# Optimization experiments

Measured on AMD Instinct MI355X. Metric: run time of the kernel, lower is better.

The kernel has to match this reference:

```python
import jax, jax.numpy as jnp
import numpy as np

B, C_IN, C_OUT = 2, 32, 32
N_IN = 128 * 128            # input grid points
N_OUT = 128 * 128           # output grid points
KERNEL_SIZE = 9             # (3-1)*4 + 1 for kernel_shape=[3,4], piecewise_linear basis
NNZ = 1_500_000             # sparse entries in psi (kernel_size, n_out, n_in)


def setup_inputs() -> dict:
    key = jax.random.key(0)
    ks = jax.random.split(key, 8)
    scale = (1.0 / C_IN) ** 0.5  # sqrt(1/groupsize), groups=1
    return {
        "x": jax.random.normal(ks[0], (B, C_IN, N_IN), jnp.float32),
        "quadrature_weights": jax.random.uniform(ks[1], (N_IN,), jnp.float32, 0.5, 1.5) / N_IN,
        "psi_vals": jax.random.uniform(ks[2], (NNZ,), jnp.float32),
        "weight": scale * jax.random.normal(ks[3], (C_OUT, C_IN, KERNEL_SIZE), jnp.float32),
        "bias": jnp.zeros((C_OUT,), jnp.float32),
        "psi_idx_k": jax.random.randint(ks[4], (NNZ,), 0, KERNEL_SIZE, dtype=jnp.int32),
        "psi_idx_out": jax.random.randint(ks[5], (NNZ,), 0, N_OUT, dtype=jnp.int32),
        "psi_idx_in": jax.random.randint(ks[6], (NNZ,), 0, N_IN, dtype=jnp.int32),
        "n_out": N_OUT,
    }


def reference(x, quadrature_weights, psi_vals, weight, bias,
              psi_idx_k, psi_idx_out, psi_idx_in, n_out):
    # x: (B, C, n_in); weight: (O, C, K); psi is sparse (K, n_out, n_in)
    Bb, C, n_in = x.shape
    K = weight.shape[2]
    # pre-multiply by quadrature weights, layout (n_in, B, C) for gather
    xq = (x * quadrature_weights[None, None, :]).transpose(2, 0, 1)
    # gather-weight: contribution of each sparse entry  -> (nnz, B, C)
    contrib = xq[psi_idx_in] * psi_vals[:, None, None]
    # scatter-add into (kernel, out) bins == sparse psi @ xq
    seg = psi_idx_k * n_out + psi_idx_out
    xk = jax.ops.segment_sum(contrib, seg, num_segments=K * n_out)
    xk = xk.reshape(K, n_out, Bb, C)  # (K, n_out, B, C)
    # channel/kernel mixing with learned weight (groups=1)
    out = jnp.einsum("knbc,ock->bon", xk, weight) + bias[None, :, None]
    return out  # (B, out_channels, n_out)
```

## Files before the change

kernel.cpp:

```cpp
#include <hip/hip_runtime.h>

#define N_IN   16384
#define N_OUT  16384
#define KSZ    9
#define CIN    32
#define COUT   32
#define BC     64
#define NBUCK  1024
#define TNB    16
#define CHUNK  4096
#define ROWS   (KSZ * TNB)
#define XSTR   64
#define ECAP   2048

__global__ void k_xq(const float* __restrict__ x, const float* __restrict__ qw,
                     float* __restrict__ xq) {
    __shared__ float tile[64 * 65];
    const int in0 = blockIdx.x * 64;
    const int tid = threadIdx.x;
#pragma unroll
    for (int i = 0; i < 16; ++i) {
        int idx = tid + i * 256;
        int bcl = idx >> 6, inl = idx & 63;
        tile[bcl * 65 + inl] = x[bcl * N_IN + in0 + inl];
    }
    __syncthreads();
#pragma unroll
    for (int i = 0; i < 16; ++i) {
        int idx = tid + i * 256;
        int inl = idx >> 6, bcl = idx & 63;
        xq[(size_t)(in0 + inl) * BC + bcl] = tile[bcl * 65 + inl] * qw[in0 + inl];
    }
}

__global__ void k_wt(const float* __restrict__ w, float* __restrict__ wT) {
    int i = blockIdx.x * 256 + threadIdx.x;
    if (i < COUT * CIN * KSZ) {
        int o = i / (CIN * KSZ);
        int r = i - o * (CIN * KSZ);
        int c = r / KSZ;
        int k = r - c * KSZ;
        wT[((k * 8 + (o >> 2)) * 32 + c) * 4 + (o & 3)] = w[i];
    }
}

__global__ __launch_bounds__(512) void k_bin(const float* __restrict__ vals,
        const int* __restrict__ ik, const int* __restrict__ io, const int* __restrict__ ii,
        int* __restrict__ gcnt, float2* __restrict__ siv, int nnz) {
    __shared__ int cnt[NBUCK];
    __shared__ int cur[NBUCK];
    __shared__ int lim[NBUCK];
    const int t = threadIdx.x, c = blockIdx.x;
    cnt[t] = 0; cnt[t + 512] = 0;
    __syncthreads();
    const int base = c * CHUNK;
    int iov[8];
#pragma unroll
    for (int j = 0; j < 8; ++j) {
        int e = base + j * 512 + t;
        iov[j] = (e < nnz) ? io[e] : -1;
        if (iov[j] >= 0) atomicAdd(&cnt[iov[j] >> 4], 1);
    }
    __syncthreads();
#pragma unroll
    for (int s = 0; s < NBUCK; s += 512) {
        int b = t + s;
        int cb = cnt[b];
        int rs = cb ? atomicAdd(&gcnt[b], cb) : 0;
        int avail = min(cb, max(0, ECAP - rs));
        cur[b] = b * ECAP + rs;
        lim[b] = b * ECAP + rs + avail;
    }
    __syncthreads();
#pragma unroll
    for (int j = 0; j < 8; ++j) {
        int e = base + j * 512 + t;
        if (iov[j] >= 0) {
            int o = iov[j], b = o >> 4;
            int packed = (ii[e] << 8) | (ik[e] * TNB + (o & (TNB - 1)));
            int pos = atomicAdd(&cur[b], 1);
            if (pos < lim[b]) siv[pos] = make_float2(vals[e], __int_as_float(packed));
        }
    }
}

__global__ __launch_bounds__(512) void k_fused3(const float* __restrict__ xq,
        const float2* __restrict__ siv, const int* __restrict__ gcnt,
        const float* __restrict__ wT, const float* __restrict__ bias,
        float* __restrict__ out) {
    __shared__ float  sxk[ROWS * XSTR];
    __shared__ float2 slist[ECAP];
    __shared__ int    rowStart[ROWS + 1];
    __shared__ int    cursor[ROWS];
    const int tid  = threadIdx.x;
    const int lane = tid & 63;
    const int wv   = __builtin_amdgcn_readfirstlane(tid >> 6);
    const int bkt  = blockIdx.x;

    for (int i = tid; i < ROWS * XSTR; i += 512) sxk[i] = 0.f;
    if (tid < ROWS) rowStart[tid] = 0;
    __syncthreads();

    const int m = min(gcnt[bkt], ECAP);
    const float2* src = siv + (size_t)bkt * ECAP;
    float2 ent[4]; bool have[4];
#pragma unroll
    for (int j = 0; j < 4; ++j) {
        int i = tid + j * 512;
        have[j] = (i < m);
        if (have[j]) {
            ent[j] = src[i];
            atomicAdd(&rowStart[__float_as_int(ent[j].y) & 0xFF], 1);
        }
    }
    __syncthreads();
    if (wv == 0) {
        int carry = 0;
#pragma unroll
        for (int i0 = 0; i0 < 192; i0 += 64) {
            int idx = i0 + lane;
            int v = (idx < ROWS) ? rowStart[idx] : 0;
            int orig = v;
#pragma unroll
            for (int off = 1; off < 64; off <<= 1) {
                int u = __shfl_up(v, off);
                if (lane >= off) v += u;
            }
            if (idx < ROWS) {
                int excl = carry + v - orig;
                rowStart[idx] = excl;
                cursor[idx]   = excl;
            }
            carry += __shfl(v, 63);
        }
        if (lane == 0) rowStart[ROWS] = m;
    }
    __syncthreads();
#pragma unroll
    for (int j = 0; j < 4; ++j) {
        if (have[j]) {
            int pos = atomicAdd(&cursor[__float_as_int(ent[j].y) & 0xFF], 1);
            slist[pos] = ent[j];
        }
    }
    __syncthreads();
    const char* xqb   = (const char*)xq;
    const int   lane4 = lane * 4;
    for (int r = wv; r < ROWS; r += 8) {
        const int a = rowStart[r], b = rowStart[r + 1];
        if (a == b) continue;
        float acc0 = 0.f, acc1 = 0.f, acc2 = 0.f, acc3 = 0.f;
        int i = a;
        for (; i + 3 < b; i += 4) {
            float2 v0 = slist[i], v1 = slist[i + 1], v2 = slist[i + 2], v3 = slist[i + 3];
            int o0 = (__float_as_int(v0.y) & 0x3FFF00) + lane4;
            int o1 = (__float_as_int(v1.y) & 0x3FFF00) + lane4;
            int o2 = (__float_as_int(v2.y) & 0x3FFF00) + lane4;
            int o3 = (__float_as_int(v3.y) & 0x3FFF00) + lane4;
            acc0 += *(const float*)(xqb + o0) * v0.x;
            acc1 += *(const float*)(xqb + o1) * v1.x;
            acc2 += *(const float*)(xqb + o2) * v2.x;
            acc3 += *(const float*)(xqb + o3) * v3.x;
        }
        for (; i < b; ++i) {
            float2 v = slist[i];
            int o = (__float_as_int(v.y) & 0x3FFF00) + lane4;
            acc0 += *(const float*)(xqb + o) * v.x;
        }
        sxk[r * XSTR + lane] = (acc0 + acc1) + (acc2 + acc3);
    }
    __syncthreads();

    if (lane < 32) {
        const int h  = lane >> 4;
        const int nl = lane & 15;
        const int n0 = bkt * TNB;
        float acc[4] = {0.f, 0.f, 0.f, 0.f};
        for (int k = 0; k < KSZ; ++k) {
            const float* xr = &sxk[(k * TNB + nl) * XSTR + h * 32];
            const float* wp = &wT[(k * 8 + wv) * 128];
#pragma unroll
            for (int c4 = 0; c4 < 8; ++c4) {
                float4 xv = *(const float4*)&xr[c4 * 4];
#pragma unroll
                for (int cc = 0; cc < 4; ++cc) {
                    float xval = (&xv.x)[cc];
#pragma unroll
                    for (int j = 0; j < 4; ++j)
                        acc[j] += xval * wp[(c4 * 4 + cc) * 4 + j];
                }
            }
        }
#pragma unroll
        for (int j = 0; j < 4; ++j) {
            int o = wv * 4 + j;
            out[((size_t)h * COUT + o) * N_OUT + n0 + nl] = acc[j] + bias[o];
        }
    }
}

extern "C" void kernel_launch(void* const* d_in, const int* in_sizes, int n_in,
                              void* d_out, int out_size, void* d_ws, size_t ws_size,
                              hipStream_t stream) {
    const float* x    = (const float*)d_in[0];
    const float* qw   = (const float*)d_in[1];
    const float* vals = (const float*)d_in[2];
    const float* w    = (const float*)d_in[3];
    const float* bias = (const float*)d_in[4];
    const int*   ik   = (const int*)d_in[5];
    const int*   io   = (const int*)d_in[6];
    const int*   ii   = (const int*)d_in[7];
    const int    nnz  = in_sizes[2];
    const int    nch  = (nnz + CHUNK - 1) / CHUNK;

    char* ws = (char*)d_ws;
    float*  xq   = (float*)ws;  ws += (size_t)N_IN * BC * 4;
    float2* siv  = (float2*)ws; ws += (size_t)NBUCK * ECAP * 8;
    int*    gcnt = (int*)ws;    ws += (size_t)NBUCK * 4;
    float*  wT   = (float*)ws;  ws += (size_t)COUT * CIN * KSZ * 4;

    hipMemsetAsync(gcnt, 0, (size_t)NBUCK * 4, stream);
    k_xq <<<N_IN / 64, 256, 0, stream>>>(x, qw, xq);
    k_wt <<<(COUT * CIN * KSZ + 255) / 256, 256, 0, stream>>>(w, wT);
    k_bin<<<nch, 512, 0, stream>>>(vals, ik, io, ii, gcnt, siv, nnz);
    k_fused3<<<NBUCK, 512, 0, stream>>>(xq, siv, gcnt, wT, bias, (float*)d_out);
}
```

Before: 184.2 us.

## Merge prep kernels, stage bucketed entries in LDS, vectorize binning loads

```diff
diff --git a/kernel.cpp b/kernel.cpp
--- a/kernel.cpp
+++ b/kernel.cpp
@@ -10,14 +10,26 @@
 #define TNB    16
 #define CHUNK  4096
 #define ROWS   (KSZ * TNB)
-#define XSTR   64
+#define XSTR   68
 #define ECAP   2048
 
 __global__ void k_xq(const float* __restrict__ x, const float* __restrict__ qw,
-                     float* __restrict__ xq) {
+                     float* __restrict__ xq, const float* __restrict__ w,
+                     float* __restrict__ wT, int* __restrict__ gcnt) {
+    const int tid = threadIdx.x;
+    if (blockIdx.x == 256) {
+        for (int i = tid; i < COUT * CIN * KSZ; i += 256) {
+            int o = i / (CIN * KSZ);
+            int r = i - o * (CIN * KSZ);
+            int c = r / KSZ;
+            int k = r - c * KSZ;
+            wT[((k * 8 + (o >> 2)) * 32 + c) * 4 + (o & 3)] = w[i];
+        }
+        for (int i = tid; i < NBUCK; i += 256) gcnt[i] = 0;
+        return;
+    }
     __shared__ float tile[64 * 65];
     const int in0 = blockIdx.x * 64;
-    const int tid = threadIdx.x;
 #pragma unroll
     for (int i = 0; i < 16; ++i) {
         int idx = tid + i * 256;
@@ -33,54 +45,94 @@
     }
 }
 
-__global__ void k_wt(const float* __restrict__ w, float* __restrict__ wT) {
-    int i = blockIdx.x * 256 + threadIdx.x;
-    if (i < COUT * CIN * KSZ) {
-        int o = i / (CIN * KSZ);
-        int r = i - o * (CIN * KSZ);
-        int c = r / KSZ;
-        int k = r - c * KSZ;
-        wT[((k * 8 + (o >> 2)) * 32 + c) * 4 + (o & 3)] = w[i];
-    }
-}
-
 __global__ __launch_bounds__(512) void k_bin(const float* __restrict__ vals,
         const int* __restrict__ ik, const int* __restrict__ io, const int* __restrict__ ii,
         int* __restrict__ gcnt, float2* __restrict__ siv, int nnz) {
-    __shared__ int cnt[NBUCK];
-    __shared__ int cur[NBUCK];
-    __shared__ int lim[NBUCK];
+    __shared__ int    cnt[NBUCK];
+    __shared__ int    gbase[NBUCK];
+    __shared__ int    cursor[NBUCK];
+    __shared__ float2 slist[CHUNK];
     const int t = threadIdx.x, c = blockIdx.x;
     cnt[t] = 0; cnt[t + 512] = 0;
     __syncthreads();
     const int base = c * CHUNK;
-    int iov[8];
+    const int e0   = base + t * 8;
+
+    float vv[8]; int pk[8]; int bk[8]; bool hv[8];
+    if (e0 + 8 <= nnz) {
+        int4 a0 = *(const int4*)(io + e0),  a1 = *(const int4*)(io + e0 + 4);
+        int4 b0 = *(const int4*)(ii + e0),  b1 = *(const int4*)(ii + e0 + 4);
+        int4 k0 = *(const int4*)(ik + e0),  k1 = *(const int4*)(ik + e0 + 4);
+        float4 d0 = *(const float4*)(vals + e0), d1 = *(const float4*)(vals + e0 + 4);
+        int ov[8] = {a0.x, a0.y, a0.z, a0.w, a1.x, a1.y, a1.z, a1.w};
+        int iv[8] = {b0.x, b0.y, b0.z, b0.w, b1.x, b1.y, b1.z, b1.w};
+        int kv[8] = {k0.x, k0.y, k0.z, k0.w, k1.x, k1.y, k1.z, k1.w};
+        float dv[8] = {d0.x, d0.y, d0.z, d0.w, d1.x, d1.y, d1.z, d1.w};
+#pragma unroll
+        for (int j = 0; j < 8; ++j) {
+            hv[j] = true;
+            bk[j] = ov[j] >> 4;
+            pk[j] = (bk[j] << 22) | (iv[j] << 8) | (kv[j] * TNB + (ov[j] & (TNB - 1)));
+            vv[j] = dv[j];
+        }
+    } else {
+#pragma unroll
+        for (int j = 0; j < 8; ++j) {
+            int e = e0 + j;
+            hv[j] = (e < nnz);
+            if (hv[j]) {
+                int o = io[e];
+                bk[j] = o >> 4;
+                pk[j] = (bk[j] << 22) | (ii[e] << 8) | (ik[e] * TNB + (o & (TNB - 1)));
+                vv[j] = vals[e];
+            } else { bk[j] = 0; pk[j] = 0; vv[j] = 0.f; }
+        }
+    }
+#pragma unroll
+    for (int j = 0; j < 8; ++j) if (hv[j]) atomicAdd(&cnt[bk[j]], 1);
+    __syncthreads();
+    {
+        int b0 = t, b1 = t + 512;
+        int c0 = cnt[b0], c1 = cnt[b1];
+        int g0 = c0 ? atomicAdd(&gcnt[b0], c0) : 0;
+        int g1 = c1 ? atomicAdd(&gcnt[b1], c1) : 0;
+        gbase[b0] = b0 * ECAP + g0;
+        gbase[b1] = b1 * ECAP + g1;
+    }
+    __syncthreads();
+    if (t < 64) {
+        int carry = 0;
+#pragma unroll
+        for (int seg = 0; seg < 16; ++seg) {
+            int idx = seg * 64 + t;
+            int v = cnt[idx];
+            int orig = v;
+#pragma unroll
+            for (int off = 1; off < 64; off <<= 1) {
+                int u = __shfl_up(v, off);
+                if (t >= off) v += u;
+            }
+            cnt[idx] = carry + v - orig;
+            carry += __shfl(v, 63);
+        }
+    }
+    __syncthreads();
+    cursor[t] = cnt[t]; cursor[t + 512] = cnt[t + 512];
+    __syncthreads();
 #pragma unroll
     for (int j = 0; j < 8; ++j) {
-        int e = base + j * 512 + t;
-        iov[j] = (e < nnz) ? io[e] : -1;
-        if (iov[j] >= 0) atomicAdd(&cnt[iov[j] >> 4], 1);
-    }
-    __syncthreads();
-#pragma unroll
-    for (int s = 0; s < NBUCK; s += 512) {
-        int b = t + s;
-        int cb = cnt[b];
-        int rs = cb ? atomicAdd(&gcnt[b], cb) : 0;
-        int avail = min(cb, max(0, ECAP - rs));
-        cur[b] = b * ECAP + rs;
-        lim[b] = b * ECAP + rs + avail;
-    }
-    __syncthreads();
-#pragma unroll
-    for (int j = 0; j < 8; ++j) {
-        int e = base + j * 512 + t;
-        if (iov[j] >= 0) {
-            int o = iov[j], b = o >> 4;
-            int packed = (ii[e] << 8) | (ik[e] * TNB + (o & (TNB - 1)));
-            int pos = atomicAdd(&cur[b], 1);
-            if (pos < lim[b]) siv[pos] = make_float2(vals[e], __int_as_float(packed));
-        }
+        if (hv[j]) {
+            int pos = atomicAdd(&cursor[bk[j]], 1);
+            slist[pos] = make_float2(vv[j], __int_as_float(pk[j]));
+        }
+    }
+    __syncthreads();
+    const int m = min(nnz - base, CHUNK);
+    for (int p = t; p < m; p += 512) {
+        float2 f = slist[p];
+        int b = (int)((unsigned)__float_as_int(f.y) >> 22);
+        int dest = gbase[b] + (p - cnt[b]);
+        if (dest < ((b + 1) << 11)) siv[dest] = f;
     }
 }
 
@@ -151,21 +203,28 @@
         if (a == b) continue;
         float acc0 = 0.f, acc1 = 0.f, acc2 = 0.f, acc3 = 0.f;
         int i = a;
+        for (; i + 7 < b; i += 8) {
+            float2 v0 = slist[i],     v1 = slist[i + 1], v2 = slist[i + 2], v3 = slist[i + 3];
+            float2 v4 = slist[i + 4], v5 = slist[i + 5], v6 = slist[i + 6], v7 = slist[i + 7];
+            acc0 += *(const float*)(xqb + ((__float_as_int(v0.y) & 0x3FFF00) + lane4)) * v0.x;
+            acc1 += *(const float*)(xqb + ((__float_as_int(v1.y) & 0x3FFF00) + lane4)) * v1.x;
+            acc2 += *(const float*)(xqb + ((__float_as_int(v2.y) & 0x3FFF00) + lane4)) * v2.x;
+            acc3 += *(const float*)(xqb + ((__float_as_int(v3.y) & 0x3FFF00) + lane4)) * v3.x;
+            acc0 += *(const float*)(xqb + ((__float_as_int(v4.y) & 0x3FFF00) + lane4)) * v4.x;
+            acc1 += *(const float*)(xqb + ((__float_as_int(v5.y) & 0x3FFF00) + lane4)) * v5.x;
+            acc2 += *(const float*)(xqb + ((__float_as_int(v6.y) & 0x3FFF00) + lane4)) * v6.x;
+            acc3 += *(const float*)(xqb + ((__float_as_int(v7.y) & 0x3FFF00) + lane4)) * v7.x;
+        }
         for (; i + 3 < b; i += 4) {
             float2 v0 = slist[i], v1 = slist[i + 1], v2 = slist[i + 2], v3 = slist[i + 3];
-            int o0 = (__float_as_int(v0.y) & 0x3FFF00) + lane4;
-            int o1 = (__float_as_int(v1.y) & 0x3FFF00) + lane4;
-            int o2 = (__float_as_int(v2.y) & 0x3FFF00) + lane4;
-            int o3 = (__float_as_int(v3.y) & 0x3FFF00) + lane4;
-            acc0 += *(const float*)(xqb + o0) * v0.x;
-            acc1 += *(const float*)(xqb + o1) * v1.x;
-            acc2 += *(const float*)(xqb + o2) * v2.x;
-            acc3 += *(const float*)(xqb + o3) * v3.x;
+            acc0 += *(const float*)(xqb + ((__float_as_int(v0.y) & 0x3FFF00) + lane4)) * v0.x;
+            acc1 += *(const float*)(xqb + ((__float_as_int(v1.y) & 0x3FFF00) + lane4)) * v1.x;
+            acc2 += *(const float*)(xqb + ((__float_as_int(v2.y) & 0x3FFF00) + lane4)) * v2.x;
+            acc3 += *(const float*)(xqb + ((__float_as_int(v3.y) & 0x3FFF00) + lane4)) * v3.x;
         }
         for (; i < b; ++i) {
             float2 v = slist[i];
-            int o = (__float_as_int(v.y) & 0x3FFF00) + lane4;
-            acc0 += *(const float*)(xqb + o) * v.x;
+            acc0 += *(const float*)(xqb + ((__float_as_int(v.y) & 0x3FFF00) + lane4)) * v.x;
         }
         sxk[r * XSTR + lane] = (acc0 + acc1) + (acc2 + acc3);
     }
@@ -219,9 +278,7 @@
     int*    gcnt = (int*)ws;    ws += (size_t)NBUCK * 4;
     float*  wT   = (float*)ws;  ws += (size_t)COUT * CIN * KSZ * 4;
 
-    hipMemsetAsync(gcnt, 0, (size_t)NBUCK * 4, stream);
-    k_xq <<<N_IN / 64, 256, 0, stream>>>(x, qw, xq);
-    k_wt <<<(COUT * CIN * KSZ + 255) / 256, 256, 0, stream>>>(w, wT);
+    k_xq <<<257, 256, 0, stream>>>(x, qw, xq, w, wT, gcnt);
     k_bin<<<nch, 512, 0, stream>>>(vals, ik, io, ii, gcnt, siv, nnz);
     k_fused3<<<NBUCK, 512, 0, stream>>>(xq, siv, gcnt, wT, bias, (float*)d_out);
 }
```

Measured after the change: 166.8 us. 1.1x faster.
